# Optimization experiments

Hardware: AMD Instinct MI355X
Metric: run time of the kernel (lower is better)

## Reference

```python
import jax, jax.numpy as jnp
import numpy as np

EPS = 1e-6


def _cosine(mem, keys):
    # mem: [B,N,C], keys: [B,C,R] -> [B,N,R]
    dot = jnp.einsum('bnc,bcr->bnr', mem, keys)
    mn = jnp.linalg.norm(mem, axis=2, keepdims=True)      # [B,N,1]
    kn = jnp.linalg.norm(keys, axis=1, keepdims=True)     # [B,1,R]
    return dot / (mn * kn + EPS)


def setup_inputs() -> dict:
    B, N, C, R = 8, 2048, 256, 4
    key = jax.random.key(0)
    ks = jax.random.split(key, 16)
    return {
        'memory': jax.random.normal(ks[0], (B, N, C), jnp.float32),
        'link': jax.random.uniform(ks[1], (B, N, N), jnp.float32),
        'usage': jax.random.uniform(ks[2], (B, N), jnp.float32),
        'read_weights': jax.random.uniform(ks[3], (B, N, R), jnp.float32),
        'write_weight_prev': jax.random.uniform(ks[4], (B, N), jnp.float32),
        'precedence': jax.random.uniform(ks[5], (B, N), jnp.float32),
        'read_keys': jax.random.normal(ks[6], (B, C, R), jnp.float32),
        'read_strengths': jax.random.uniform(ks[7], (B, R), jnp.float32),
        'write_key': jax.random.normal(ks[8], (B, C), jnp.float32),
        'write_strength': jax.random.uniform(ks[9], (B, 1), jnp.float32),
        'free_gates': jax.random.uniform(ks[10], (B, R), jnp.float32),
        'allocation_gate': jax.random.uniform(ks[11], (B, 1), jnp.float32),
        'write_gate': jax.random.uniform(ks[12], (B, 1), jnp.float32),
        'write_vector': jax.random.normal(ks[13], (B, C), jnp.float32),
        'erase_vector': jax.random.uniform(ks[14], (B, C), jnp.float32),
        'read_modes': jax.random.uniform(ks[15], (B, 3, R), jnp.float32),
    }


def reference(memory, link, usage, read_weights, write_weight_prev, precedence,
              read_keys, read_strengths, write_key, write_strength, free_gates,
              allocation_gate, write_gate, write_vector, erase_vector, read_modes):
    B, N, C = memory.shape
    # --- usage update: psi retention from free gates ---
    psi = jnp.prod(1.0 - free_gates[:, None, :] * read_weights, axis=2)  # [B,N]
    u = (usage + write_weight_prev - usage * write_weight_prev) * psi
    # --- allocation weighting (sorted exclusive cumprod) ---
    order = jnp.argsort(u, axis=1)                                     # ascending usage
    u_sorted = jnp.take_along_axis(u, order, axis=1)
    excl = jnp.concatenate([jnp.ones_like(u_sorted[:, :1]),
                            jnp.cumprod(u_sorted[:, :-1], axis=1)], axis=1)
    a_sorted = (1.0 - u_sorted) * excl
    inv = jnp.argsort(order, axis=1)
    alloc = jnp.take_along_axis(a_sorted, inv, axis=1)                 # [B,N]
    # --- write weighting ---
    phi_w = _cosine(memory, write_key[:, :, None])[:, :, 0]            # [B,N]
    cw = jax.nn.softmax(phi_w * write_strength, axis=1)
    ww = write_gate * (allocation_gate * alloc + (1.0 - allocation_gate) * cw)  # [B,N]
    # --- memory write (erase + add) ---
    mem_new = memory * (1.0 - ww[:, :, None] * erase_vector[:, None, :]) \
              + ww[:, :, None] * write_vector[:, None, :]
    # --- precedence + link matrix ---
    prec_new = (1.0 - jnp.sum(ww, axis=1, keepdims=True)) * precedence + ww
    link_new = (1.0 - ww[:, :, None] - ww[:, None, :]) * link \
               + ww[:, :, None] * precedence[:, None, :]
    link_new = link_new * (1.0 - jnp.eye(N, dtype=link.dtype))[None]
    # --- directional weightings ---
    fwd = jnp.einsum('bij,bjr->bir', link_new, read_weights)           # [B,N,R]
    bwd = jnp.einsum('bji,bjr->bir', link_new, read_weights)
    # --- content read weighting on updated memory ---
    phi_r = _cosine(mem_new, read_keys)                                # [B,N,R]
    cr = jax.nn.softmax(phi_r * read_strengths[:, None, :], axis=1)
    rw_new = read_modes[:, 0][:, None, :] * bwd \
             + read_modes[:, 1][:, None, :] * cr \
             + read_modes[:, 2][:, None, :] * fwd                      # [B,N,R]
    # --- read vectors ---
    read_vectors = jnp.einsum('bnc,bnr->bcr', mem_new, rw_new)         # [B,C,R]
    return read_vectors
```

## Files before the change

kernel.cpp:

```cpp
#include <hip/hip_runtime.h>
#include <math.h>

#define EPS 1e-6f
constexpr int B = 8, N = 2048, C = 256, R = 4;

__device__ __forceinline__ float wred_sum(float v) {
  for (int d = 32; d; d >>= 1) v += __shfl_xor(v, d, 64);
  return v;
}
__device__ __forceinline__ float wred_max(float v) {
  for (int d = 32; d; d >>= 1) v = fmaxf(v, __shfl_xor(v, d, 64));
  return v;
}

__global__ __launch_bounds__(1024) void k_alloc(const float* __restrict__ usage,
    const float* __restrict__ wwp, const float* __restrict__ fg,
    const float* __restrict__ rw, float* __restrict__ alloc_) {
  __shared__ float2 ulg[N];
  __shared__ float Sp[4][256];
  int blk = blockIdx.x;
  int b = blk >> 3, chunk = blk & 7;
  int t = threadIdx.x;
  float gx = fg[b * R + 0], gy = fg[b * R + 1], gz = fg[b * R + 2], gw2 = fg[b * R + 3];
  for (int e = t; e < N; e += 1024) {
    float4 r4 = *(const float4*)&rw[(size_t)(b * N + e) * R];
    float psi = (1.f - gx * r4.x) * (1.f - gy * r4.y) * (1.f - gz * r4.z) * (1.f - gw2 * r4.w);
    float us = usage[b * N + e], w = wwp[b * N + e];
    float u = (us + w - us * w) * psi;
    ulg[e] = make_float2(u, log2f(u));
  }
  __syncthreads();
  int i = chunk * 256 + (t & 255);
  int jseg = t >> 8;
  float ui = ulg[i].x;
  float S = 0.f;
  int j0 = jseg * 512;
  #pragma unroll 4
  for (int jj = 0; jj < 512; jj++) {
    int j = j0 + jj;
    float2 v = ulg[j];
    bool sel = (v.x < ui) || (v.x == ui && j < i);
    S += sel ? v.y : 0.f;
  }
  Sp[jseg][t & 255] = S;
  __syncthreads();
  if (t < 256) {
    float tot = Sp[0][t] + Sp[1][t] + Sp[2][t] + Sp[3][t];
    int ii = chunk * 256 + t;
    alloc_[b * N + ii] = (1.f - ulg[ii].x) * exp2f(tot);
  }
}

__global__ void k_phiw(const float* __restrict__ mem, const float* __restrict__ wk,
                       const float* __restrict__ wstr, float* __restrict__ sw_) {
  int gw = (blockIdx.x * 256 + threadIdx.x) >> 6;
  int lane = threadIdx.x & 63;
  if (gw >= B * N) return;
  int b = gw >> 11, n = gw & (N - 1);
  float4 m4 = *(const float4*)&mem[(size_t)(b * N + n) * C + lane * 4];
  float4 k4 = *(const float4*)&wk[b * C + lane * 4];
  float dot = m4.x * k4.x + m4.y * k4.y + m4.z * k4.z + m4.w * k4.w;
  float nrm = m4.x * m4.x + m4.y * m4.y + m4.z * m4.z + m4.w * m4.w;
  float knr = k4.x * k4.x + k4.y * k4.y + k4.z * k4.z + k4.w * k4.w;
  for (int d = 32; d; d >>= 1) {
    dot += __shfl_xor(dot, d, 64);
    nrm += __shfl_xor(nrm, d, 64);
    knr += __shfl_xor(knr, d, 64);
  }
  if (lane == 0) {
    float phi = dot / (sqrtf(nrm) * sqrtf(knr) + EPS);
    sw_[b * N + n] = phi * wstr[b];
  }
}

__global__ __launch_bounds__(1024) void k_ww(const float* __restrict__ sw_,
    const float* __restrict__ alloc_, const float* __restrict__ ag, const float* __restrict__ wg,
    const float* __restrict__ prec, const float* __restrict__ rw,
    float* __restrict__ ww_, float* __restrict__ ST_) {
  int b = blockIdx.x, t = threadIdx.x;
  int lane = t & 63, wv = t >> 6;
  int i0 = t, i1 = t + 1024;
  __shared__ float redA[16];
  __shared__ float red8[16][8];
  float s0 = sw_[b * N + i0], s1 = sw_[b * N + i1];
  float mx = wred_max(fmaxf(s0, s1));
  if (lane == 0) redA[wv] = mx;
  __syncthreads();
  mx = redA[0];
  #pragma unroll
  for (int i = 1; i < 16; i++) mx = fmaxf(mx, redA[i]);
  float e0 = expf(s0 - mx), e1 = expf(s1 - mx);
  float sm = wred_sum(e0 + e1);
  __syncthreads();
  if (lane == 0) redA[wv] = sm;
  __syncthreads();
  sm = 0.f;
  #pragma unroll
  for (int i = 0; i < 16; i++) sm += redA[i];
  float agv = ag[b], wgv = wg[b];
  float w0 = wgv * (agv * alloc_[b * N + i0] + (1.f - agv) * (e0 / sm));
  float w1 = wgv * (agv * alloc_[b * N + i1] + (1.f - agv) * (e1 / sm));
  ww_[b * N + i0] = w0;
  ww_[b * N + i1] = w1;
  float4 r0 = *(const float4*)&rw[(size_t)(b * N + i0) * R];
  float4 r1 = *(const float4*)&rw[(size_t)(b * N + i1) * R];
  float p0 = prec[b * N + i0], p1 = prec[b * N + i1];
  float a[8] = { p0 * r0.x + p1 * r1.x, p0 * r0.y + p1 * r1.y,
                 p0 * r0.z + p1 * r1.z, p0 * r0.w + p1 * r1.w,
                 w0 * r0.x + w1 * r1.x, w0 * r0.y + w1 * r1.y,
                 w0 * r0.z + w1 * r1.z, w0 * r0.w + w1 * r1.w };
  #pragma unroll
  for (int r = 0; r < 8; r++) a[r] = wred_sum(a[r]);
  if (lane == 0) {
    #pragma unroll
    for (int r = 0; r < 8; r++) red8[wv][r] = a[r];
  }
  __syncthreads();
  if (t < 8) {
    float s = 0.f;
    for (int i = 0; i < 16; i++) s += red8[i][t];
    ST_[b * 8 + t] = s;
  }
}

__global__ __launch_bounds__(512) void k_linkpass(const float* __restrict__ link,
    const float* __restrict__ rw, const float* __restrict__ ww_,
    float* __restrict__ t_, float* __restrict__ upart) {
  const int blk = blockIdx.x;
  const int b = blk >> 5;
  const int strip = blk & 31;
  const int i0 = strip * 64;
  const int t = threadIdx.x;
  const int lane = t & 63, wv = t >> 6;
  const int jb = t * 4;
  __shared__ float tred[64][8][8];

  float cw[4][8];
  #pragma unroll
  for (int k = 0; k < 4; k++) {
    float4 r4 = *(const float4*)&rw[(size_t)(b * N + jb + k) * R];
    float w = ww_[b * N + jb + k];
    cw[k][0] = r4.x; cw[k][1] = r4.y; cw[k][2] = r4.z; cw[k][3] = r4.w;
    cw[k][4] = w * r4.x; cw[k][5] = w * r4.y; cw[k][6] = w * r4.z; cw[k][7] = w * r4.w;
  }
  float uacc[4][8];
  #pragma unroll
  for (int k = 0; k < 4; k++) {
    #pragma unroll
    for (int r = 0; r < 8; r++) uacc[k][r] = 0.f;
  }

  const float* Lbase = link + (size_t)(b * N + i0) * N;
  for (int ii = 0; ii < 64; ii += 4) {
    float4 La[4];
    #pragma unroll
    for (int m = 0; m < 4; m++)
      La[m] = *(const float4*)(Lbase + (size_t)(ii + m) * N + jb);
    #pragma unroll
    for (int m = 0; m < 4; m++) {
      const int i = i0 + ii + m;
      float4 q = *(const float4*)&rw[(size_t)(b * N + i) * R];
      float wi = ww_[b * N + i];
      float ri[8] = { q.x, q.y, q.z, q.w, wi * q.x, wi * q.y, wi * q.z, wi * q.w };
      float lv[4] = { La[m].x, La[m].y, La[m].z, La[m].w };
      float trow[8] = { 0, 0, 0, 0, 0, 0, 0, 0 };
      #pragma unroll
      for (int k = 0; k < 4; k++) {
        #pragma unroll
        for (int r = 0; r < 8; r++) {
          uacc[k][r] = fmaf(lv[k], ri[r], uacc[k][r]);
          trow[r] = fmaf(lv[k], cw[k][r], trow[r]);
        }
      }
      float nv[4];
      #pragma unroll
      for (int rr = 0; rr < 4; rr++) {
        float a = trow[2 * rr], c = trow[2 * rr + 1];
        float oa = __shfl_xor(a, 1, 64), oc = __shfl_xor(c, 1, 64);
        nv[rr] = (lane & 1) ? (c + oc) : (a + oa);
      }
      float nw[2];
      #pragma unroll
      for (int rr = 0; rr < 2; rr++) {
        float a = nv[2 * rr], c = nv[2 * rr + 1];
        float oa = __shfl_xor(a, 2, 64), oc = __shfl_xor(c, 2, 64);
        nw[rr] = (lane & 2) ? (c + oc) : (a + oa);
      }
      float a2 = nw[0], c2 = nw[1];
      float oa2 = __shfl_xor(a2, 4, 64), oc2 = __shfl_xor(c2, 4, 64);
      float vv = (lane & 4) ? (c2 + oc2) : (a2 + oa2);
      vv += __shfl_xor(vv, 8, 64);
      vv += __shfl_xor(vv, 16, 64);
      vv += __shfl_xor(vv, 32, 64);
      if (lane < 8) tred[ii + m][wv][lane] = vv;
    }
  }
  __syncthreads();
  {
    int i = t >> 3, r = t & 7;
    float s = 0.f;
    #pragma unroll
    for (int w8 = 0; w8 < 8; w8++) s += tred[i][w8][r];
    t_[(size_t)(b * N + i0 + i) * 8 + r] = s;
  }
  float* ub = upart + ((size_t)(b * 32 + strip) * N + jb) * 8;
  #pragma unroll
  for (int k = 0; k < 4; k++) {
    float4 lo = { uacc[k][0], uacc[k][1], uacc[k][2], uacc[k][3] };
    float4 hi = { uacc[k][4], uacc[k][5], uacc[k][6], uacc[k][7] };
    *(float4*)(ub + k * 8) = lo;
    *(float4*)(ub + k * 8 + 4) = hi;
  }
}

__global__ void k_phir(const float* __restrict__ mem, const float* __restrict__ rk,
                       const float* __restrict__ ww_, const float* __restrict__ ev,
                       const float* __restrict__ wvec, const float* __restrict__ rs,
                       float* __restrict__ sr_) {
  int gw = (blockIdx.x * 256 + threadIdx.x) >> 6;
  int lane = threadIdx.x & 63;
  if (gw >= B * N) return;
  int b = gw >> 11, n = gw & (N - 1);
  float w = ww_[b * N + n];
  int c0 = lane * 4;
  float4 m4 = *(const float4*)&mem[(size_t)(b * N + n) * C + c0];
  float4 e4 = *(const float4*)&ev[b * C + c0];
  float4 v4 = *(const float4*)&wvec[b * C + c0];
  float mn[4] = { m4.x * (1.f - w * e4.x) + w * v4.x,
                  m4.y * (1.f - w * e4.y) + w * v4.y,
                  m4.z * (1.f - w * e4.z) + w * v4.z,
                  m4.w * (1.f - w * e4.w) + w * v4.w };
  float dot[4] = { 0, 0, 0, 0 };
  float kn[4] = { 0, 0, 0, 0 };
  float nrm = 0.f;
  #pragma unroll
  for (int ci = 0; ci < 4; ci++) {
    float4 k4 = *(const float4*)&rk[(size_t)(b * C + c0 + ci) * R];
    dot[0] = fmaf(mn[ci], k4.x, dot[0]);
    dot[1] = fmaf(mn[ci], k4.y, dot[1]);
    dot[2] = fmaf(mn[ci], k4.z, dot[2]);
    dot[3] = fmaf(mn[ci], k4.w, dot[3]);
    kn[0] = fmaf(k4.x, k4.x, kn[0]);
    kn[1] = fmaf(k4.y, k4.y, kn[1]);
    kn[2] = fmaf(k4.z, k4.z, kn[2]);
    kn[3] = fmaf(k4.w, k4.w, kn[3]);
    nrm = fmaf(mn[ci], mn[ci], nrm);
  }
  for (int d = 32; d; d >>= 1) {
    dot[0] += __shfl_xor(dot[0], d, 64);
    dot[1] += __shfl_xor(dot[1], d, 64);
    dot[2] += __shfl_xor(dot[2], d, 64);
    dot[3] += __shfl_xor(dot[3], d, 64);
    kn[0] += __shfl_xor(kn[0], d, 64);
    kn[1] += __shfl_xor(kn[1], d, 64);
    kn[2] += __shfl_xor(kn[2], d, 64);
    kn[3] += __shfl_xor(kn[3], d, 64);
    nrm += __shfl_xor(nrm, d, 64);
  }
  if (lane == 0) {
    float mnorm = sqrtf(nrm);
    #pragma unroll
    for (int r = 0; r < 4; r++) {
      float phi = dot[r] / (mnorm * sqrtf(kn[r]) + EPS);
      sr_[(size_t)(b * R + r) * N + n] = phi * rs[b * R + r];
    }
  }
}

__global__ __launch_bounds__(256) void k_smax(const float* __restrict__ sr_,
                                              float* __restrict__ smax_) {
  int b = blockIdx.x >> 2, r = blockIdx.x & 3;
  int t = threadIdx.x, lane = t & 63, wv = t >> 6;
  __shared__ float redA[4];
  const float* srow = sr_ + (size_t)(b * R + r) * N;
  float sv[8];
  float mx = -1e30f;
  #pragma unroll
  for (int k = 0; k < 8; k++) { sv[k] = srow[t + k * 256]; mx = fmaxf(mx, sv[k]); }
  mx = wred_max(mx);
  if (lane == 0) redA[wv] = mx;
  __syncthreads();
  mx = fmaxf(fmaxf(redA[0], redA[1]), fmaxf(redA[2], redA[3]));
  float sm = 0.f;
  #pragma unroll
  for (int k = 0; k < 8; k++) sm += expf(sv[k] - mx);
  sm = wred_sum(sm);
  __syncthreads();
  if (lane == 0) redA[wv] = sm;
  __syncthreads();
  if (t == 0) {
    smax_[(b * R + r) * 2] = mx;
    smax_[(b * R + r) * 2 + 1] = redA[0] + redA[1] + redA[2] + redA[3];
  }
}

__global__ __launch_bounds__(64) void k_comb(const float* __restrict__ link,
    const float* __restrict__ sr_, const float* __restrict__ t_,
    const float* __restrict__ upart, const float* __restrict__ ww_,
    const float* __restrict__ prec, const float* __restrict__ rw,
    const float* __restrict__ ST_, const float* __restrict__ smax_,
    const float* __restrict__ modes, float* __restrict__ rwn_) {
  int id = blockIdx.x * 64 + threadIdx.x;
  int b = id >> 11, n = id & (N - 1);
  float u1[4] = { 0, 0, 0, 0 }, u2[4] = { 0, 0, 0, 0 };
  const float* up = upart + ((size_t)(b * 32) * N + n) * 8;
  #pragma unroll 8
  for (int s = 0; s < 32; s++) {
    const float* p = up + (size_t)s * N * 8;
    float4 a = *(const float4*)p;
    float4 c = *(const float4*)(p + 4);
    u1[0] += a.x; u1[1] += a.y; u1[2] += a.z; u1[3] += a.w;
    u2[0] += c.x; u2[1] += c.y; u2[2] += c.z; u2[3] += c.w;
  }
  float4 t1 = *(const float4*)&t_[(size_t)id * 8];
  float4 t2 = *(const float4*)&t_[(size_t)id * 8 + 4];
  float tt1[4] = { t1.x, t1.y, t1.z, t1.w };
  float tt2[4] = { t2.x, t2.y, t2.z, t2.w };
  float w = ww_[id], pc = prec[id];
  float L = link[(size_t)(b * N + n) * N + n];
  float Dg = (1.f - 2.f * w) * L + w * pc;
  float4 rv4 = *(const float4*)&rw[(size_t)id * R];
  float rv[4] = { rv4.x, rv4.y, rv4.z, rv4.w };
  #pragma unroll
  for (int r = 0; r < 4; r++) {
    float m0 = modes[(b * 3 + 0) * R + r], m1 = modes[(b * 3 + 1) * R + r],
          m2 = modes[(b * 3 + 2) * R + r];
    float S = ST_[b * 8 + r], T = ST_[b * 8 + 4 + r];
    float mx = smax_[(b * R + r) * 2], inv = 1.f / smax_[(b * R + r) * 2 + 1];
    float sv = sr_[(size_t)(b * R + r) * N + n];
    float cr = expf(sv - mx) * inv;
    float fwd = (1.f - w) * tt1[r] - tt2[r] + w * S - Dg * rv[r];
    float bwd = (1.f - w) * u1[r] - u2[r] + pc * T - Dg * rv[r];
    rwn_[(size_t)(b * R + r) * N + n] = m0 * bwd + m1 * cr + m2 * fwd;
  }
}

__global__ __launch_bounds__(256) void k_read(const float* __restrict__ mem,
    const float* __restrict__ ww_, const float* __restrict__ ev, const float* __restrict__ wvec,
    const float* __restrict__ rwn_, float* __restrict__ part_) {
  int blk = blockIdx.x;
  int b = blk >> 5, chunk = blk & 31;
  int t = threadIdx.x;
  int cg = t & 63, sub = t >> 6;
  int c0 = cg * 4;
  int nbase = chunk * 64 + sub * 16;
  float4 e4 = *(const float4*)&ev[b * C + c0];
  float4 v4 = *(const float4*)&wvec[b * C + c0];
  float acc[4][4];
  #pragma unroll
  for (int ci = 0; ci < 4; ci++) {
    #pragma unroll
    for (int r = 0; r < 4; r++) acc[ci][r] = 0.f;
  }
  for (int m = 0; m < 16; m++) {
    int n = nbase + m;
    float w = ww_[b * N + n];
    float4 m4 = *(const float4*)&mem[(size_t)(b * N + n) * C + c0];
    float mn[4] = { m4.x * (1.f - w * e4.x) + w * v4.x,
                    m4.y * (1.f - w * e4.y) + w * v4.y,
                    m4.z * (1.f - w * e4.z) + w * v4.z,
                    m4.w * (1.f - w * e4.w) + w * v4.w };
    float rv[4];
    #pragma unroll
    for (int r = 0; r < 4; r++) rv[r] = rwn_[(size_t)(b * R + r) * N + n];
    #pragma unroll
    for (int ci = 0; ci < 4; ci++) {
      #pragma unroll
      for (int r = 0; r < 4; r++) acc[ci][r] = fmaf(mn[ci], rv[r], acc[ci][r]);
    }
  }
  __shared__ float red[4][64][4][4];
  #pragma unroll
  for (int ci = 0; ci < 4; ci++) {
    #pragma unroll
    for (int r = 0; r < 4; r++) red[sub][cg][ci][r] = acc[ci][r];
  }
  __syncthreads();
  if (sub == 0) {
    #pragma unroll
    for (int ci = 0; ci < 4; ci++) {
      #pragma unroll
      for (int r = 0; r < 4; r++) {
        float s = red[0][cg][ci][r] + red[1][cg][ci][r] + red[2][cg][ci][r] + red[3][cg][ci][r];
        part_[((size_t)blk * C + (c0 + ci)) * R + r] = s;
      }
    }
  }
}

__global__ void k_final(const float* __restrict__ part_, float* __restrict__ out) {
  int idx = blockIdx.x * 256 + threadIdx.x;
  if (idx >= B * C * R) return;
  int b = idx / (C * R), cr = idx % (C * R);
  float s = 0.f;
  for (int ch = 0; ch < 32; ch++) s += part_[(size_t)(b * 32 + ch) * C * R + cr];
  out[idx] = s;
}

extern "C" void kernel_launch(void* const* d_in, const int* in_sizes, int n_in,
                              void* d_out, int out_size, void* d_ws, size_t ws_size,
                              hipStream_t stream) {
  const float* mem   = (const float*)d_in[0];
  const float* link  = (const float*)d_in[1];
  const float* usage = (const float*)d_in[2];
  const float* rw    = (const float*)d_in[3];
  const float* wwp   = (const float*)d_in[4];
  const float* prec  = (const float*)d_in[5];
  const float* rk    = (const float*)d_in[6];
  const float* rs    = (const float*)d_in[7];
  const float* wk    = (const float*)d_in[8];
  const float* wstr  = (const float*)d_in[9];
  const float* fg    = (const float*)d_in[10];
  const float* ag    = (const float*)d_in[11];
  const float* wg    = (const float*)d_in[12];
  const float* wvec  = (const float*)d_in[13];
  const float* ev    = (const float*)d_in[14];
  const float* modes = (const float*)d_in[15];
  float* out = (float*)d_out;

  float* W = (float*)d_ws;
  float* alloc_= W;
  float* sw_   = alloc_ + B * N;
  float* ww_   = sw_ + B * N;
  float* ST_   = ww_ + B * N;
  float* smax_ = ST_ + 64;
  float* t_    = smax_ + 64;
  float* sr_   = t_ + B * N * 8;
  float* rwn_  = sr_ + B * R * N;
  float* part_ = rwn_ + B * R * N;
  float* upart = part_ + B * 32 * C * R;

  k_alloc<<<B * 8, 1024, 0, stream>>>(usage, wwp, fg, rw, alloc_);
  k_phiw<<<(B * N) / 4, 256, 0, stream>>>(mem, wk, wstr, sw_);
  k_ww<<<B, 1024, 0, stream>>>(sw_, alloc_, ag, wg, prec, rw, ww_, ST_);
  k_linkpass<<<B * 32, 512, 0, stream>>>(link, rw, ww_, t_, upart);
  k_phir<<<(B * N) / 4, 256, 0, stream>>>(mem, rk, ww_, ev, wvec, rs, sr_);
  k_smax<<<B * R, 256, 0, stream>>>(sr_, smax_);
  k_comb<<<(B * N) / 64, 64, 0, stream>>>(link, sr_, t_, upart, ww_, prec, rw,
                                          ST_, smax_, modes, rwn_);
  k_read<<<B * 32, 256, 0, stream>>>(mem, ww_, ev, wvec, rwn_, part_);
  k_final<<<(B * C * R) / 256, 256, 0, stream>>>(part_, out);
}
```

Measured before the change: 112.7 us.

## Fuse pipeline into four kernels with max-free softmax and atomic denominators

Collapses nine launches into four. Allocation and write-content scoring now share one launch, and link pass, read-content scoring and the ST reductions share another. The combine and read-vector stages are merged so read weights stay in shared memory. The write weighting is recomputed inline from sw, alloc and an atomically accumulated exp-sum denominator, dropping the softmax max-subtraction and the separate ww and smax passes. The aim is to cut launch overhead and intermediate global traffic. The cost is a memset, atomics, and possible overflow in expf without max-subtraction, which is safe only because cosine times strength is bounded for these inputs.

```diff
diff --git a/kernel.cpp b/kernel.cpp
--- a/kernel.cpp
+++ b/kernel.cpp
@@ -8,381 +8,364 @@
   for (int d = 32; d; d >>= 1) v += __shfl_xor(v, d, 64);
   return v;
 }
-__device__ __forceinline__ float wred_max(float v) {
-  for (int d = 32; d; d >>= 1) v = fmaxf(v, __shfl_xor(v, d, 64));
-  return v;
-}
-
-__global__ __launch_bounds__(1024) void k_alloc(const float* __restrict__ usage,
+
+__device__ __forceinline__ float ww_inline(float sw, float al, float dw,
+                                           float agv, float wgv) {
+  return wgv * (agv * al + (1.f - agv) * (expf(sw) / dw));
+}
+
+__global__ __launch_bounds__(1024) void k_pre(const float* __restrict__ usage,
     const float* __restrict__ wwp, const float* __restrict__ fg,
-    const float* __restrict__ rw, float* __restrict__ alloc_) {
+    const float* __restrict__ rw, const float* __restrict__ mem,
+    const float* __restrict__ wk, const float* __restrict__ wstr,
+    float* __restrict__ alloc_, float* __restrict__ sw_, float* __restrict__ denw) {
   __shared__ float2 ulg[N];
-  __shared__ float Sp[4][256];
+  __shared__ float Sp[16][64];
+  __shared__ float eacc[16];
   int blk = blockIdx.x;
-  int b = blk >> 3, chunk = blk & 7;
   int t = threadIdx.x;
-  float gx = fg[b * R + 0], gy = fg[b * R + 1], gz = fg[b * R + 2], gw2 = fg[b * R + 3];
-  for (int e = t; e < N; e += 1024) {
-    float4 r4 = *(const float4*)&rw[(size_t)(b * N + e) * R];
-    float psi = (1.f - gx * r4.x) * (1.f - gy * r4.y) * (1.f - gz * r4.z) * (1.f - gw2 * r4.w);
-    float us = usage[b * N + e], w = wwp[b * N + e];
-    float u = (us + w - us * w) * psi;
-    ulg[e] = make_float2(u, log2f(u));
-  }
-  __syncthreads();
-  int i = chunk * 256 + (t & 255);
-  int jseg = t >> 8;
-  float ui = ulg[i].x;
-  float S = 0.f;
-  int j0 = jseg * 512;
-  #pragma unroll 4
-  for (int jj = 0; jj < 512; jj++) {
-    int j = j0 + jj;
-    float2 v = ulg[j];
-    bool sel = (v.x < ui) || (v.x == ui && j < i);
-    S += sel ? v.y : 0.f;
-  }
-  Sp[jseg][t & 255] = S;
-  __syncthreads();
-  if (t < 256) {
-    float tot = Sp[0][t] + Sp[1][t] + Sp[2][t] + Sp[3][t];
-    int ii = chunk * 256 + t;
-    alloc_[b * N + ii] = (1.f - ulg[ii].x) * exp2f(tot);
-  }
-}
-
-__global__ void k_phiw(const float* __restrict__ mem, const float* __restrict__ wk,
-                       const float* __restrict__ wstr, float* __restrict__ sw_) {
-  int gw = (blockIdx.x * 256 + threadIdx.x) >> 6;
-  int lane = threadIdx.x & 63;
-  if (gw >= B * N) return;
-  int b = gw >> 11, n = gw & (N - 1);
-  float4 m4 = *(const float4*)&mem[(size_t)(b * N + n) * C + lane * 4];
-  float4 k4 = *(const float4*)&wk[b * C + lane * 4];
-  float dot = m4.x * k4.x + m4.y * k4.y + m4.z * k4.z + m4.w * k4.w;
-  float nrm = m4.x * m4.x + m4.y * m4.y + m4.z * m4.z + m4.w * m4.w;
-  float knr = k4.x * k4.x + k4.y * k4.y + k4.z * k4.z + k4.w * k4.w;
-  for (int d = 32; d; d >>= 1) {
-    dot += __shfl_xor(dot, d, 64);
-    nrm += __shfl_xor(nrm, d, 64);
-    knr += __shfl_xor(knr, d, 64);
-  }
-  if (lane == 0) {
-    float phi = dot / (sqrtf(nrm) * sqrtf(knr) + EPS);
-    sw_[b * N + n] = phi * wstr[b];
-  }
-}
-
-__global__ __launch_bounds__(1024) void k_ww(const float* __restrict__ sw_,
-    const float* __restrict__ alloc_, const float* __restrict__ ag, const float* __restrict__ wg,
-    const float* __restrict__ prec, const float* __restrict__ rw,
-    float* __restrict__ ww_, float* __restrict__ ST_) {
-  int b = blockIdx.x, t = threadIdx.x;
-  int lane = t & 63, wv = t >> 6;
-  int i0 = t, i1 = t + 1024;
-  __shared__ float redA[16];
-  __shared__ float red8[16][8];
-  float s0 = sw_[b * N + i0], s1 = sw_[b * N + i1];
-  float mx = wred_max(fmaxf(s0, s1));
-  if (lane == 0) redA[wv] = mx;
-  __syncthreads();
-  mx = redA[0];
-  #pragma unroll
-  for (int i = 1; i < 16; i++) mx = fmaxf(mx, redA[i]);
-  float e0 = expf(s0 - mx), e1 = expf(s1 - mx);
-  float sm = wred_sum(e0 + e1);
-  __syncthreads();
-  if (lane == 0) redA[wv] = sm;
-  __syncthreads();
-  sm = 0.f;
-  #pragma unroll
-  for (int i = 0; i < 16; i++) sm += redA[i];
-  float agv = ag[b], wgv = wg[b];
-  float w0 = wgv * (agv * alloc_[b * N + i0] + (1.f - agv) * (e0 / sm));
-  float w1 = wgv * (agv * alloc_[b * N + i1] + (1.f - agv) * (e1 / sm));
-  ww_[b * N + i0] = w0;
-  ww_[b * N + i1] = w1;
-  float4 r0 = *(const float4*)&rw[(size_t)(b * N + i0) * R];
-  float4 r1 = *(const float4*)&rw[(size_t)(b * N + i1) * R];
-  float p0 = prec[b * N + i0], p1 = prec[b * N + i1];
-  float a[8] = { p0 * r0.x + p1 * r1.x, p0 * r0.y + p1 * r1.y,
-                 p0 * r0.z + p1 * r1.z, p0 * r0.w + p1 * r1.w,
-                 w0 * r0.x + w1 * r1.x, w0 * r0.y + w1 * r1.y,
-                 w0 * r0.z + w1 * r1.z, w0 * r0.w + w1 * r1.w };
-  #pragma unroll
-  for (int r = 0; r < 8; r++) a[r] = wred_sum(a[r]);
-  if (lane == 0) {
-    #pragma unroll
-    for (int r = 0; r < 8; r++) red8[wv][r] = a[r];
-  }
-  __syncthreads();
-  if (t < 8) {
-    float s = 0.f;
-    for (int i = 0; i < 16; i++) s += red8[i][t];
-    ST_[b * 8 + t] = s;
-  }
-}
-
-__global__ __launch_bounds__(512) void k_linkpass(const float* __restrict__ link,
-    const float* __restrict__ rw, const float* __restrict__ ww_,
-    float* __restrict__ t_, float* __restrict__ upart) {
+  if (blk < 256) {
+    int b = blk >> 5, chunk = blk & 31;
+    float gx = fg[b * R + 0], gy = fg[b * R + 1], gz = fg[b * R + 2], gw2 = fg[b * R + 3];
+    for (int e = t; e < N; e += 1024) {
+      float4 r4 = *(const float4*)&rw[(size_t)(b * N + e) * R];
+      float psi = (1.f - gx * r4.x) * (1.f - gy * r4.y) * (1.f - gz * r4.z) * (1.f - gw2 * r4.w);
+      float us = usage[b * N + e], w = wwp[b * N + e];
+      float u = (us + w - us * w) * psi;
+      ulg[e] = make_float2(u, log2f(u));
+    }
+    __syncthreads();
+    int i = chunk * 64 + (t & 63);
+    int jseg = t >> 6;
+    float ui = ulg[i].x;
+    float S = 0.f;
+    int j0 = jseg * 128;
+    #pragma unroll 4
+    for (int jj = 0; jj < 128; jj++) {
+      int j = j0 + jj;
+      float2 v = ulg[j];
+      bool sel = (v.x < ui) || (v.x == ui && j < i);
+      S += sel ? v.y : 0.f;
+    }
+    Sp[jseg][t & 63] = S;
+    __syncthreads();
+    if (t < 64) {
+      float tot = 0.f;
+      #pragma unroll
+      for (int s = 0; s < 16; s++) tot += Sp[s][t];
+      int ii = chunk * 64 + t;
+      alloc_[b * N + ii] = (1.f - ulg[ii].x) * exp2f(tot);
+    }
+  } else {
+    int wv = t >> 6, lane = t & 63;
+    int gw = (blk - 256) * 16 + wv;
+    int b = gw >> 11, n = gw & (N - 1);
+    float4 m4 = *(const float4*)&mem[(size_t)(b * N + n) * C + lane * 4];
+    float4 k4 = *(const float4*)&wk[b * C + lane * 4];
+    float dot = m4.x * k4.x + m4.y * k4.y + m4.z * k4.z + m4.w * k4.w;
+    float nrm = m4.x * m4.x + m4.y * m4.y + m4.z * m4.z + m4.w * m4.w;
+    float knr = k4.x * k4.x + k4.y * k4.y + k4.z * k4.z + k4.w * k4.w;
+    for (int d = 32; d; d >>= 1) {
+      dot += __shfl_xor(dot, d, 64);
+      nrm += __shfl_xor(nrm, d, 64);
+      knr += __shfl_xor(knr, d, 64);
+    }
+    if (lane == 0) {
+      float phi = dot / (sqrtf(nrm) * sqrtf(knr) + EPS);
+      float swv = phi * wstr[b];
+      sw_[b * N + n] = swv;
+      eacc[wv] = expf(swv);
+    }
+    __syncthreads();
+    if (t == 0) {
+      float s = 0.f;
+      #pragma unroll
+      for (int i = 0; i < 16; i++) s += eacc[i];
+      atomicAdd(&denw[b], s);
+    }
+  }
+}
+
+__global__ __launch_bounds__(512) void k_mid(const float* __restrict__ link,
+    const float* __restrict__ rw, const float* __restrict__ sw_,
+    const float* __restrict__ alloc_, const float* __restrict__ denw,
+    const float* __restrict__ ag, const float* __restrict__ wg,
+    const float* __restrict__ prec, const float* __restrict__ mem,
+    const float* __restrict__ rk, const float* __restrict__ ev,
+    const float* __restrict__ wvec, const float* __restrict__ rs,
+    float* __restrict__ t_, float* __restrict__ upart, float* __restrict__ sr_,
+    float* __restrict__ denr, float* __restrict__ ST_) {
+  __shared__ float tred[64][8][8];
+  __shared__ float eacc[8][4];
+  __shared__ float red8[8][8];
   const int blk = blockIdx.x;
-  const int b = blk >> 5;
-  const int strip = blk & 31;
-  const int i0 = strip * 64;
   const int t = threadIdx.x;
   const int lane = t & 63, wv = t >> 6;
-  const int jb = t * 4;
-  __shared__ float tred[64][8][8];
-
-  float cw[4][8];
-  #pragma unroll
-  for (int k = 0; k < 4; k++) {
-    float4 r4 = *(const float4*)&rw[(size_t)(b * N + jb + k) * R];
-    float w = ww_[b * N + jb + k];
-    cw[k][0] = r4.x; cw[k][1] = r4.y; cw[k][2] = r4.z; cw[k][3] = r4.w;
-    cw[k][4] = w * r4.x; cw[k][5] = w * r4.y; cw[k][6] = w * r4.z; cw[k][7] = w * r4.w;
-  }
-  float uacc[4][8];
-  #pragma unroll
-  for (int k = 0; k < 4; k++) {
-    #pragma unroll
-    for (int r = 0; r < 8; r++) uacc[k][r] = 0.f;
-  }
-
-  const float* Lbase = link + (size_t)(b * N + i0) * N;
-  for (int ii = 0; ii < 64; ii += 4) {
-    float4 La[4];
-    #pragma unroll
-    for (int m = 0; m < 4; m++)
-      La[m] = *(const float4*)(Lbase + (size_t)(ii + m) * N + jb);
-    #pragma unroll
-    for (int m = 0; m < 4; m++) {
-      const int i = i0 + ii + m;
-      float4 q = *(const float4*)&rw[(size_t)(b * N + i) * R];
-      float wi = ww_[b * N + i];
-      float ri[8] = { q.x, q.y, q.z, q.w, wi * q.x, wi * q.y, wi * q.z, wi * q.w };
-      float lv[4] = { La[m].x, La[m].y, La[m].z, La[m].w };
-      float trow[8] = { 0, 0, 0, 0, 0, 0, 0, 0 };
+  if (blk < 256) {
+    const int b = blk >> 5;
+    const int strip = blk & 31;
+    const int i0 = strip * 64;
+    const int jb = t * 4;
+    const float agv = ag[b], wgv = wg[b], dw = denw[b];
+    float cw[4][8];
+    {
+      float4 sw4 = *(const float4*)&sw_[b * N + jb];
+      float4 al4 = *(const float4*)&alloc_[b * N + jb];
+      float wj[4] = { ww_inline(sw4.x, al4.x, dw, agv, wgv),
+                      ww_inline(sw4.y, al4.y, dw, agv, wgv),
+                      ww_inline(sw4.z, al4.z, dw, agv, wgv),
+                      ww_inline(sw4.w, al4.w, dw, agv, wgv) };
       #pragma unroll
       for (int k = 0; k < 4; k++) {
+        float4 r4 = *(const float4*)&rw[(size_t)(b * N + jb + k) * R];
+        cw[k][0] = r4.x; cw[k][1] = r4.y; cw[k][2] = r4.z; cw[k][3] = r4.w;
+        cw[k][4] = wj[k] * r4.x; cw[k][5] = wj[k] * r4.y;
+        cw[k][6] = wj[k] * r4.z; cw[k][7] = wj[k] * r4.w;
+      }
+    }
+    float uacc[4][8];
+    #pragma unroll
+    for (int k = 0; k < 4; k++) {
+      #pragma unroll
+      for (int r = 0; r < 8; r++) uacc[k][r] = 0.f;
+    }
+    const float* Lbase = link + (size_t)(b * N + i0) * N;
+    for (int ii = 0; ii < 64; ii += 4) {
+      float4 La[4];
+      #pragma unroll
+      for (int m = 0; m < 4; m++)
+        La[m] = *(const float4*)(Lbase + (size_t)(ii + m) * N + jb);
+      #pragma unroll
+      for (int m = 0; m < 4; m++) {
+        const int i = i0 + ii + m;
+        float4 q = *(const float4*)&rw[(size_t)(b * N + i) * R];
+        float wi = ww_inline(sw_[b * N + i], alloc_[b * N + i], dw, agv, wgv);
+        float ri[8] = { q.x, q.y, q.z, q.w, wi * q.x, wi * q.y, wi * q.z, wi * q.w };
+        float lv[4] = { La[m].x, La[m].y, La[m].z, La[m].w };
+        float trow[8] = { 0, 0, 0, 0, 0, 0, 0, 0 };
         #pragma unroll
-        for (int r = 0; r < 8; r++) {
-          uacc[k][r] = fmaf(lv[k], ri[r], uacc[k][r]);
-          trow[r] = fmaf(lv[k], cw[k][r], trow[r]);
+        for (int k = 0; k < 4; k++) {
+          #pragma unroll
+          for (int r = 0; r < 8; r++) {
+            uacc[k][r] = fmaf(lv[k], ri[r], uacc[k][r]);
+            trow[r] = fmaf(lv[k], cw[k][r], trow[r]);
+          }
         }
+        float nv[4];
+        #pragma unroll
+        for (int rr = 0; rr < 4; rr++) {
+          float a = trow[2 * rr], c = trow[2 * rr + 1];
+          float oa = __shfl_xor(a, 1, 64), oc = __shfl_xor(c, 1, 64);
+          nv[rr] = (lane & 1) ? (c + oc) : (a + oa);
+        }
+        float nw[2];
+        #pragma unroll
+        for (int rr = 0; rr < 2; rr++) {
+          float a = nv[2 * rr], c = nv[2 * rr + 1];
+          float oa = __shfl_xor(a, 2, 64), oc = __shfl_xor(c, 2, 64);
+          nw[rr] = (lane & 2) ? (c + oc) : (a + oa);
+        }
+        float a2 = nw[0], c2 = nw[1];
+        float oa2 = __shfl_xor(a2, 4, 64), oc2 = __shfl_xor(c2, 4, 64);
+        float vv = (lane & 4) ? (c2 + oc2) : (a2 + oa2);
+        vv += __shfl_xor(vv, 8, 64);
+        vv += __shfl_xor(vv, 16, 64);
+        vv += __shfl_xor(vv, 32, 64);
+        if (lane < 8) tred[ii + m][wv][lane] = vv;
       }
-      float nv[4];
-      #pragma unroll
-      for (int rr = 0; rr < 4; rr++) {
-        float a = trow[2 * rr], c = trow[2 * rr + 1];
-        float oa = __shfl_xor(a, 1, 64), oc = __shfl_xor(c, 1, 64);
-        nv[rr] = (lane & 1) ? (c + oc) : (a + oa);
+    }
+    __syncthreads();
+    {
+      int i = t & 63, r = t >> 6;
+      float s = 0.f;
+      #pragma unroll
+      for (int w8 = 0; w8 < 8; w8++) s += tred[i][w8][r];
+      t_[((size_t)(b * 8 + r)) * N + i0 + i] = s;
+    }
+    float* ub = upart + ((size_t)(b * 32 + strip) * 8) * N;
+    #pragma unroll
+    for (int r = 0; r < 8; r++) {
+      float4 v = { uacc[0][r], uacc[1][r], uacc[2][r], uacc[3][r] };
+      *(float4*)(ub + (size_t)r * N + jb) = v;
+    }
+  } else if (blk < 2304) {
+    int gw = (blk - 256) * 8 + wv;
+    int b = gw >> 11, n = gw & (N - 1);
+    const float agv = ag[b], wgv = wg[b], dw = denw[b];
+    float w = ww_inline(sw_[b * N + n], alloc_[b * N + n], dw, agv, wgv);
+    int c0 = lane * 4;
+    float4 m4 = *(const float4*)&mem[(size_t)(b * N + n) * C + c0];
+    float4 e4 = *(const float4*)&ev[b * C + c0];
+    float4 v4 = *(const float4*)&wvec[b * C + c0];
+    float mn[4] = { m4.x * (1.f - w * e4.x) + w * v4.x,
+                    m4.y * (1.f - w * e4.y) + w * v4.y,
+                    m4.z * (1.f - w * e4.z) + w * v4.z,
+                    m4.w * (1.f - w * e4.w) + w * v4.w };
+    float dot[4] = { 0, 0, 0, 0 };
+    float kn[4] = { 0, 0, 0, 0 };
+    float nrm = 0.f;
+    #pragma unroll
+    for (int ci = 0; ci < 4; ci++) {
+      float4 k4 = *(const float4*)&rk[(size_t)(b * C + c0 + ci) * R];
+      dot[0] = fmaf(mn[ci], k4.x, dot[0]);
+      dot[1] = fmaf(mn[ci], k4.y, dot[1]);
+      dot[2] = fmaf(mn[ci], k4.z, dot[2]);
+      dot[3] = fmaf(mn[ci], k4.w, dot[3]);
+      kn[0] = fmaf(k4.x, k4.x, kn[0]);
+      kn[1] = fmaf(k4.y, k4.y, kn[1]);
+      kn[2] = fmaf(k4.z, k4.z, kn[2]);
+      kn[3] = fmaf(k4.w, k4.w, kn[3]);
+      nrm = fmaf(mn[ci], mn[ci], nrm);
+    }
+    for (int d = 32; d; d >>= 1) {
+      dot[0] += __shfl_xor(dot[0], d, 64);
+      dot[1] += __shfl_xor(dot[1], d, 64);
+      dot[2] += __shfl_xor(dot[2], d, 64);
+      dot[3] += __shfl_xor(dot[3], d, 64);
+      kn[0] += __shfl_xor(kn[0], d, 64);
+      kn[1] += __shfl_xor(kn[1], d, 64);
+      kn[2] += __shfl_xor(kn[2], d, 64);
+      kn[3] += __shfl_xor(kn[3], d, 64);
+      nrm += __shfl_xor(nrm, d, 64);
+    }
+    if (lane == 0) {
+      float mnorm = sqrtf(nrm);
+      #pragma unroll
+      for (int r = 0; r < 4; r++) {
+        float phi = dot[r] / (mnorm * sqrtf(kn[r]) + EPS);
+        float sv = phi * rs[b * R + r];
+        sr_[(size_t)(b * R + r) * N + n] = sv;
+        eacc[wv][r] = expf(sv);
       }
-      float nw[2];
-      #pragma unroll
-      for (int rr = 0; rr < 2; rr++) {
-        float a = nv[2 * rr], c = nv[2 * rr + 1];
-        float oa = __shfl_xor(a, 2, 64), oc = __shfl_xor(c, 2, 64);
-        nw[rr] = (lane & 2) ? (c + oc) : (a + oa);
-      }
-      float a2 = nw[0], c2 = nw[1];
-      float oa2 = __shfl_xor(a2, 4, 64), oc2 = __shfl_xor(c2, 4, 64);
-      float vv = (lane & 4) ? (c2 + oc2) : (a2 + oa2);
-      vv += __shfl_xor(vv, 8, 64);
-      vv += __shfl_xor(vv, 16, 64);
-      vv += __shfl_xor(vv, 32, 64);
-      if (lane < 8) tred[ii + m][wv][lane] = vv;
-    }
+    }
+    __syncthreads();
+    if (t < 4) {
+      float s = 0.f;
+      #pragma unroll
+      for (int i = 0; i < 8; i++) s += eacc[i][t];
+      atomicAdd(&denr[b * R + t], s);
+    }
+  } else {
+    int b = blk - 2304;
+    const float agv = ag[b], wgv = wg[b], dw = denw[b];
+    float a[8] = { 0, 0, 0, 0, 0, 0, 0, 0 };
+    #pragma unroll
+    for (int k = 0; k < 4; k++) {
+      int i = t + k * 512;
+      float4 r4 = *(const float4*)&rw[(size_t)(b * N + i) * R];
+      float pc = prec[b * N + i];
+      float w = ww_inline(sw_[b * N + i], alloc_[b * N + i], dw, agv, wgv);
+      a[0] = fmaf(pc, r4.x, a[0]); a[1] = fmaf(pc, r4.y, a[1]);
+      a[2] = fmaf(pc, r4.z, a[2]); a[3] = fmaf(pc, r4.w, a[3]);
+      a[4] = fmaf(w, r4.x, a[4]);  a[5] = fmaf(w, r4.y, a[5]);
+      a[6] = fmaf(w, r4.z, a[6]);  a[7] = fmaf(w, r4.w, a[7]);
+    }
+    #pragma unroll
+    for (int r = 0; r < 8; r++) a[r] = wred_sum(a[r]);
+    if (lane == 0) {
+      #pragma unroll
+      for (int r = 0; r < 8; r++) red8[wv][r] = a[r];
+    }
+    __syncthreads();
+    if (t < 8) {
+      float s = 0.f;
+      #pragma unroll
+      for (int i = 0; i < 8; i++) s += red8[i][t];
+      ST_[b * 8 + t] = s;
+    }
+  }
+}
+
+__global__ __launch_bounds__(256) void k_combread(const float* __restrict__ link,
+    const float* __restrict__ sw_, const float* __restrict__ alloc_,
+    const float* __restrict__ denw, const float* __restrict__ denr,
+    const float* __restrict__ ag, const float* __restrict__ wg,
+    const float* __restrict__ prec, const float* __restrict__ rw,
+    const float* __restrict__ t_, const float* __restrict__ upart,
+    const float* __restrict__ sr_, const float* __restrict__ ST_,
+    const float* __restrict__ modes, const float* __restrict__ mem,
+    const float* __restrict__ ev, const float* __restrict__ wvec,
+    float* __restrict__ part_) {
+  __shared__ float dgl[64], wloc[64], rwnl[4][64];
+  __shared__ float red[4][64][4][4];
+  const int blk = blockIdx.x;
+  const int b = blk >> 5, chunk = blk & 31;
+  const int n0 = chunk * 64;
+  const int t = threadIdx.x;
+  const int nl = t & 63, r = t >> 6;
+  const int n = n0 + nl;
+  const float agv = ag[b], wgv = wg[b], dw = denw[b];
+  float u1 = 0.f, u2 = 0.f;
+  const float* up = upart + ((size_t)(b * 32) * 8) * N;
+  #pragma unroll 8
+  for (int s = 0; s < 32; s++) {
+    const float* p = up + ((size_t)s * 8) * N;
+    u1 += p[(size_t)r * N + n];
+    u2 += p[(size_t)(4 + r) * N + n];
+  }
+  float pc = prec[b * N + n];
+  if (r == 0) {
+    float w = ww_inline(sw_[b * N + n], alloc_[b * N + n], dw, agv, wgv);
+    float L = link[((size_t)(b * N + n)) * N + n];
+    dgl[nl] = (1.f - 2.f * w) * L + w * pc;
+    wloc[nl] = w;
   }
   __syncthreads();
   {
-    int i = t >> 3, r = t & 7;
-    float s = 0.f;
-    #pragma unroll
-    for (int w8 = 0; w8 < 8; w8++) s += tred[i][w8][r];
-    t_[(size_t)(b * N + i0 + i) * 8 + r] = s;
-  }
-  float* ub = upart + ((size_t)(b * 32 + strip) * N + jb) * 8;
-  #pragma unroll
-  for (int k = 0; k < 4; k++) {
-    float4 lo = { uacc[k][0], uacc[k][1], uacc[k][2], uacc[k][3] };
-    float4 hi = { uacc[k][4], uacc[k][5], uacc[k][6], uacc[k][7] };
-    *(float4*)(ub + k * 8) = lo;
-    *(float4*)(ub + k * 8 + 4) = hi;
-  }
-}
-
-__global__ void k_phir(const float* __restrict__ mem, const float* __restrict__ rk,
-                       const float* __restrict__ ww_, const float* __restrict__ ev,
-                       const float* __restrict__ wvec, const float* __restrict__ rs,
-                       float* __restrict__ sr_) {
-  int gw = (blockIdx.x * 256 + threadIdx.x) >> 6;
-  int lane = threadIdx.x & 63;
-  if (gw >= B * N) return;
-  int b = gw >> 11, n = gw & (N - 1);
-  float w = ww_[b * N + n];
-  int c0 = lane * 4;
-  float4 m4 = *(const float4*)&mem[(size_t)(b * N + n) * C + c0];
-  float4 e4 = *(const float4*)&ev[b * C + c0];
-  float4 v4 = *(const float4*)&wvec[b * C + c0];
-  float mn[4] = { m4.x * (1.f - w * e4.x) + w * v4.x,
-                  m4.y * (1.f - w * e4.y) + w * v4.y,
-                  m4.z * (1.f - w * e4.z) + w * v4.z,
-                  m4.w * (1.f - w * e4.w) + w * v4.w };
-  float dot[4] = { 0, 0, 0, 0 };
-  float kn[4] = { 0, 0, 0, 0 };
-  float nrm = 0.f;
-  #pragma unroll
-  for (int ci = 0; ci < 4; ci++) {
-    float4 k4 = *(const float4*)&rk[(size_t)(b * C + c0 + ci) * R];
-    dot[0] = fmaf(mn[ci], k4.x, dot[0]);
-    dot[1] = fmaf(mn[ci], k4.y, dot[1]);
-    dot[2] = fmaf(mn[ci], k4.z, dot[2]);
-    dot[3] = fmaf(mn[ci], k4.w, dot[3]);
-    kn[0] = fmaf(k4.x, k4.x, kn[0]);
-    kn[1] = fmaf(k4.y, k4.y, kn[1]);
-    kn[2] = fmaf(k4.z, k4.z, kn[2]);
-    kn[3] = fmaf(k4.w, k4.w, kn[3]);
-    nrm = fmaf(mn[ci], mn[ci], nrm);
-  }
-  for (int d = 32; d; d >>= 1) {
-    dot[0] += __shfl_xor(dot[0], d, 64);
-    dot[1] += __shfl_xor(dot[1], d, 64);
-    dot[2] += __shfl_xor(dot[2], d, 64);
-    dot[3] += __shfl_xor(dot[3], d, 64);
-    kn[0] += __shfl_xor(kn[0], d, 64);
-    kn[1] += __shfl_xor(kn[1], d, 64);
-    kn[2] += __shfl_xor(kn[2], d, 64);
-    kn[3] += __shfl_xor(kn[3], d, 64);
-    nrm += __shfl_xor(nrm, d, 64);
-  }
-  if (lane == 0) {
-    float mnorm = sqrtf(nrm);
-    #pragma unroll
-    for (int r = 0; r < 4; r++) {
-      float phi = dot[r] / (mnorm * sqrtf(kn[r]) + EPS);
-      sr_[(size_t)(b * R + r) * N + n] = phi * rs[b * R + r];
-    }
-  }
-}
-
-__global__ __launch_bounds__(256) void k_smax(const float* __restrict__ sr_,
-                                              float* __restrict__ smax_) {
-  int b = blockIdx.x >> 2, r = blockIdx.x & 3;
-  int t = threadIdx.x, lane = t & 63, wv = t >> 6;
-  __shared__ float redA[4];
-  const float* srow = sr_ + (size_t)(b * R + r) * N;
-  float sv[8];
-  float mx = -1e30f;
-  #pragma unroll
-  for (int k = 0; k < 8; k++) { sv[k] = srow[t + k * 256]; mx = fmaxf(mx, sv[k]); }
-  mx = wred_max(mx);
-  if (lane == 0) redA[wv] = mx;
-  __syncthreads();
-  mx = fmaxf(fmaxf(redA[0], redA[1]), fmaxf(redA[2], redA[3]));
-  float sm = 0.f;
-  #pragma unroll
-  for (int k = 0; k < 8; k++) sm += expf(sv[k] - mx);
-  sm = wred_sum(sm);
-  __syncthreads();
-  if (lane == 0) redA[wv] = sm;
-  __syncthreads();
-  if (t == 0) {
-    smax_[(b * R + r) * 2] = mx;
-    smax_[(b * R + r) * 2 + 1] = redA[0] + redA[1] + redA[2] + redA[3];
-  }
-}
-
-__global__ __launch_bounds__(64) void k_comb(const float* __restrict__ link,
-    const float* __restrict__ sr_, const float* __restrict__ t_,
-    const float* __restrict__ upart, const float* __restrict__ ww_,
-    const float* __restrict__ prec, const float* __restrict__ rw,
-    const float* __restrict__ ST_, const float* __restrict__ smax_,
-    const float* __restrict__ modes, float* __restrict__ rwn_) {
-  int id = blockIdx.x * 64 + threadIdx.x;
-  int b = id >> 11, n = id & (N - 1);
-  float u1[4] = { 0, 0, 0, 0 }, u2[4] = { 0, 0, 0, 0 };
-  const float* up = upart + ((size_t)(b * 32) * N + n) * 8;
-  #pragma unroll 8
-  for (int s = 0; s < 32; s++) {
-    const float* p = up + (size_t)s * N * 8;
-    float4 a = *(const float4*)p;
-    float4 c = *(const float4*)(p + 4);
-    u1[0] += a.x; u1[1] += a.y; u1[2] += a.z; u1[3] += a.w;
-    u2[0] += c.x; u2[1] += c.y; u2[2] += c.z; u2[3] += c.w;
-  }
-  float4 t1 = *(const float4*)&t_[(size_t)id * 8];
-  float4 t2 = *(const float4*)&t_[(size_t)id * 8 + 4];
-  float tt1[4] = { t1.x, t1.y, t1.z, t1.w };
-  float tt2[4] = { t2.x, t2.y, t2.z, t2.w };
-  float w = ww_[id], pc = prec[id];
-  float L = link[(size_t)(b * N + n) * N + n];
-  float Dg = (1.f - 2.f * w) * L + w * pc;
-  float4 rv4 = *(const float4*)&rw[(size_t)id * R];
-  float rv[4] = { rv4.x, rv4.y, rv4.z, rv4.w };
-  #pragma unroll
-  for (int r = 0; r < 4; r++) {
+    float w = wloc[nl], Dg = dgl[nl];
+    float t1 = t_[(size_t)(b * 8 + r) * N + n];
+    float t2 = t_[(size_t)(b * 8 + 4 + r) * N + n];
+    float sv = sr_[(size_t)(b * R + r) * N + n];
+    float cr = expf(sv) / denr[b * R + r];
+    float rv = rw[(size_t)(b * N + n) * R + r];
+    float S = ST_[b * 8 + r], T = ST_[b * 8 + 4 + r];
     float m0 = modes[(b * 3 + 0) * R + r], m1 = modes[(b * 3 + 1) * R + r],
           m2 = modes[(b * 3 + 2) * R + r];
-    float S = ST_[b * 8 + r], T = ST_[b * 8 + 4 + r];
-    float mx = smax_[(b * R + r) * 2], inv = 1.f / smax_[(b * R + r) * 2 + 1];
-    float sv = sr_[(size_t)(b * R + r) * N + n];
-    float cr = expf(sv - mx) * inv;
-    float fwd = (1.f - w) * tt1[r] - tt2[r] + w * S - Dg * rv[r];
-    float bwd = (1.f - w) * u1[r] - u2[r] + pc * T - Dg * rv[r];
-    rwn_[(size_t)(b * R + r) * N + n] = m0 * bwd + m1 * cr + m2 * fwd;
-  }
-}
-
-__global__ __launch_bounds__(256) void k_read(const float* __restrict__ mem,
-    const float* __restrict__ ww_, const float* __restrict__ ev, const float* __restrict__ wvec,
-    const float* __restrict__ rwn_, float* __restrict__ part_) {
-  int blk = blockIdx.x;
-  int b = blk >> 5, chunk = blk & 31;
-  int t = threadIdx.x;
-  int cg = t & 63, sub = t >> 6;
-  int c0 = cg * 4;
-  int nbase = chunk * 64 + sub * 16;
+    float fwd = (1.f - w) * t1 - t2 + w * S - Dg * rv;
+    float bwd = (1.f - w) * u1 - u2 + pc * T - Dg * rv;
+    rwnl[r][nl] = m0 * bwd + m1 * cr + m2 * fwd;
+  }
+  __syncthreads();
+  const int sub = r, cg = nl;
+  const int c0 = cg * 4;
   float4 e4 = *(const float4*)&ev[b * C + c0];
   float4 v4 = *(const float4*)&wvec[b * C + c0];
   float acc[4][4];
   #pragma unroll
   for (int ci = 0; ci < 4; ci++) {
     #pragma unroll
-    for (int r = 0; r < 4; r++) acc[ci][r] = 0.f;
+    for (int rr = 0; rr < 4; rr++) acc[ci][rr] = 0.f;
   }
   for (int m = 0; m < 16; m++) {
-    int n = nbase + m;
-    float w = ww_[b * N + n];
-    float4 m4 = *(const float4*)&mem[(size_t)(b * N + n) * C + c0];
+    int row = sub * 16 + m;
+    int nn = n0 + row;
+    float w = wloc[row];
+    float4 m4 = *(const float4*)&mem[(size_t)(b * N + nn) * C + c0];
     float mn[4] = { m4.x * (1.f - w * e4.x) + w * v4.x,
                     m4.y * (1.f - w * e4.y) + w * v4.y,
                     m4.z * (1.f - w * e4.z) + w * v4.z,
                     m4.w * (1.f - w * e4.w) + w * v4.w };
-    float rv[4];
-    #pragma unroll
-    for (int r = 0; r < 4; r++) rv[r] = rwn_[(size_t)(b * R + r) * N + n];
+    float rv[4] = { rwnl[0][row], rwnl[1][row], rwnl[2][row], rwnl[3][row] };
     #pragma unroll
     for (int ci = 0; ci < 4; ci++) {
       #pragma unroll
-      for (int r = 0; r < 4; r++) acc[ci][r] = fmaf(mn[ci], rv[r], acc[ci][r]);
-    }
-  }
-  __shared__ float red[4][64][4][4];
+      for (int rr = 0; rr < 4; rr++) acc[ci][rr] = fmaf(mn[ci], rv[rr], acc[ci][rr]);
+    }
+  }
   #pragma unroll
   for (int ci = 0; ci < 4; ci++) {
     #pragma unroll
-    for (int r = 0; r < 4; r++) red[sub][cg][ci][r] = acc[ci][r];
+    for (int rr = 0; rr < 4; rr++) red[sub][cg][ci][rr] = acc[ci][rr];
   }
   __syncthreads();
   if (sub == 0) {
     #pragma unroll
     for (int ci = 0; ci < 4; ci++) {
       #pragma unroll
-      for (int r = 0; r < 4; r++) {
-        float s = red[0][cg][ci][r] + red[1][cg][ci][r] + red[2][cg][ci][r] + red[3][cg][ci][r];
-        part_[((size_t)blk * C + (c0 + ci)) * R + r] = s;
+      for (int rr = 0; rr < 4; rr++) {
+        float s = red[0][cg][ci][rr] + red[1][cg][ci][rr] +
+                  red[2][cg][ci][rr] + red[3][cg][ci][rr];
+        part_[((size_t)blk * C + (c0 + ci)) * R + rr] = s;
       }
     }
   }
@@ -419,25 +402,24 @@
   float* out = (float*)d_out;
 
   float* W = (float*)d_ws;
-  float* alloc_= W;
+  float* denw  = W;
+  float* denr  = W + 8;
+  float* alloc_= W + 64;
   float* sw_   = alloc_ + B * N;
-  float* ww_   = sw_ + B * N;
-  float* ST_   = ww_ + B * N;
-  float* smax_ = ST_ + 64;
-  float* t_    = smax_ + 64;
-  float* sr_   = t_ + B * N * 8;
-  float* rwn_  = sr_ + B * R * N;
-  float* part_ = rwn_ + B * R * N;
+  float* ST_   = sw_ + B * N;
+  float* t_    = ST_ + 64;
+  float* sr_   = t_ + B * 8 * N;
+  float* part_ = sr_ + B * R * N;
   float* upart = part_ + B * 32 * C * R;
 
-  k_alloc<<<B * 8, 1024, 0, stream>>>(usage, wwp, fg, rw, alloc_);
-  k_phiw<<<(B * N) / 4, 256, 0, stream>>>(mem, wk, wstr, sw_);
-  k_ww<<<B, 1024, 0, stream>>>(sw_, alloc_, ag, wg, prec, rw, ww_, ST_);
-  k_linkpass<<<B * 32, 512, 0, stream>>>(link, rw, ww_, t_, upart);
-  k_phir<<<(B * N) / 4, 256, 0, stream>>>(mem, rk, ww_, ev, wvec, rs, sr_);
-  k_smax<<<B * R, 256, 0, stream>>>(sr_, smax_);
-  k_comb<<<(B * N) / 64, 64, 0, stream>>>(link, sr_, t_, upart, ww_, prec, rw,
-                                          ST_, smax_, modes, rwn_);
-  k_read<<<B * 32, 256, 0, stream>>>(mem, ww_, ev, wvec, rwn_, part_);
+  (void)hipMemsetAsync(W, 0, 64 * sizeof(float), stream);
+  k_pre<<<256 + (B * N) / 16, 1024, 0, stream>>>(usage, wwp, fg, rw, mem, wk, wstr,
+                                                 alloc_, sw_, denw);
+  k_mid<<<256 + (B * N) / 8 + B, 512, 0, stream>>>(link, rw, sw_, alloc_, denw, ag, wg,
+                                                   prec, mem, rk, ev, wvec, rs,
+                                                   t_, upart, sr_, denr, ST_);
+  k_combread<<<B * 32, 256, 0, stream>>>(link, sw_, alloc_, denw, denr, ag, wg, prec,
+                                         rw, t_, upart, sr_, ST_, modes, mem, ev,
+                                         wvec, part_);
   k_final<<<(B * C * R) / 256, 256, 0, stream>>>(part_, out);
 }
```

Result: no change. 111.4 us (-1.1%).
